# Performance work log

Measured on AMD Instinct MI355X. Metric: run time of the kernel, lower is better.

Reference implementation:

```python
import jax, jax.numpy as jnp
import numpy as np

# Model hyperparameters (from init_kwargs)
B, N, D = 64, 196, 768      # batch, patches, patch_dim
TKN = 768                   # token dim
QK = 64                     # per-head qk dim
H = 12                      # heads
HN = int(4.0 * TKN)         # Hopfield hidden = 3072
BETA = 1.0 / np.sqrt(QK)    # attn_beta default: 1/sqrt(qk_dim)
BLOCKS = 2
K_STEPS = 4                 # time_steps per block
EPS = 1e-5
ALPHA_RAW0 = float(np.log(np.exp(1.0) - 1.0))  # softplus^-1(alpha_init=1.0)


def setup_inputs() -> dict:
    key = jax.random.key(0)
    ks = jax.random.split(key, 8)
    sd = 0.02
    return {
        "x": jax.random.normal(ks[0], (B, N, D), dtype=jnp.float32),
        "W_enc": jax.random.normal(ks[1], (D, TKN), dtype=jnp.float32) * sd,
        "b_enc": jnp.zeros((TKN,), jnp.float32),
        "cls": jnp.ones((1, 1, TKN), jnp.float32),
        "pos": jax.random.normal(ks[2], (1, N + 1, TKN), dtype=jnp.float32) * sd,
        "gamma": jnp.ones((BLOCKS,), jnp.float32),             # EnergyLayerNorm scalar gain per block
        "bias": jnp.zeros((BLOCKS, TKN), jnp.float32),          # EnergyLayerNorm bias per block
        "Wq": jax.random.normal(ks[3], (BLOCKS, H, QK, TKN), dtype=jnp.float32) * sd,
        "Wk": jax.random.normal(ks[4], (BLOCKS, H, QK, TKN), dtype=jnp.float32) * sd,
        "Whn": jax.random.normal(ks[5], (BLOCKS, TKN, HN), dtype=jnp.float32) * sd,
        "alpha_raw": jnp.full((BLOCKS,), ALPHA_RAW0, jnp.float32),
        "ln_g": jnp.ones((TKN,), jnp.float32),
        "ln_b": jnp.zeros((TKN,), jnp.float32),
        "W_dec": jax.random.normal(ks[6], (TKN, D), dtype=jnp.float32) * sd,
        "b_dec": jnp.zeros((D,), jnp.float32),
    }


def _enorm(x, g_scale, g_bias):
    # EnergyLayerNorm: scalar gamma, per-dim bias, RMS of centered x
    xm = x - x.mean(-1, keepdims=True)
    return g_scale * xm * jax.lax.rsqrt((xm * xm).mean(-1, keepdims=True) + EPS) + g_bias


def _energy(g, Wq, Wk, Whn):
    # Hopfield-attention energy: -1/beta * sum logsumexp(beta * K^T Q)
    q = jnp.einsum("bnd,hzd->bnhz", g, Wq)
    k = jnp.einsum("bnd,hzd->bnhz", g, Wk)
    logits = jnp.einsum("bqhz,bkhz->bhqk", q, k)  # [B,H,N+1,N+1]
    e_attn = -(1.0 / BETA) * jnp.sum(jax.nn.logsumexp(BETA * logits, axis=-1))
    # Hopfield memory energy: -0.5 * sum relu(g W)^2
    e_hn = -0.5 * jnp.sum(jax.nn.relu(g @ Whn) ** 2)
    return e_attn + e_hn


_egrad = jax.grad(_energy)


def reference(x, W_enc, b_enc, cls, pos, gamma, bias, Wq, Wk, Whn, alpha_raw,
              ln_g, ln_b, W_dec, b_dec):
    t = x @ W_enc + b_enc                                   # encode -> [B,N,TKN]
    t = jnp.concatenate([jnp.broadcast_to(cls, (t.shape[0], 1, TKN)), t], axis=1)
    t = t + pos                                             # [B,N+1,TKN]
    for b in range(BLOCKS):
        a = jax.nn.softplus(alpha_raw[b])
        for _ in range(K_STEPS):
            g = _enorm(t, gamma[b], bias[b])
            t = t - a * _egrad(g, Wq[b], Wk[b], Whn[b])
    # decode: standard LayerNorm then Linear
    mu = t.mean(-1, keepdims=True)
    var = ((t - mu) ** 2).mean(-1, keepdims=True)
    h = (t - mu) * jax.lax.rsqrt(var + EPS) * ln_g + ln_b
    out = h @ W_dec + b_dec
    return out[:, 1:]                                       # drop CLS -> [B,N,D]
```

## Files before the change

kernel.cpp:

```cpp
#include <hip/hip_runtime.h>
#include <cstdint>
#include <cstddef>

using u16 = unsigned short;
typedef short short8 __attribute__((ext_vector_type(8)));
typedef short short4v __attribute__((ext_vector_type(4)));
typedef float f32x4 __attribute__((ext_vector_type(4)));

#define LN_EPS 1e-5f
#define ATT_BETA 0.125f

__device__ __forceinline__ u16 f2bf(float f){
  uint32_t u = __float_as_uint(f);
  u += 0x7fffu + ((u >> 16) & 1u);
  return (u16)(u >> 16);
}
__device__ __forceinline__ float bf2f(u16 h){
  return __uint_as_float(((uint32_t)h) << 16);
}
__device__ __forceinline__ float wred_sum(float v){
  #pragma unroll
  for(int o=32;o;o>>=1) v += __shfl_xor(v,o,64);
  return v;
}
__device__ __forceinline__ void async16(const void* g, void* l){
  __builtin_amdgcn_global_load_lds((const __attribute__((address_space(1))) void*)g,
                                   (__attribute__((address_space(3))) void*)l, 16, 0, 0);
}

template<int EPI, int ASPL>
__global__ __launch_bounds__(256)
void gemm_bt(const u16* __restrict__ A, const u16* __restrict__ A2,
             const u16* __restrict__ B,
             u16* __restrict__ Cb, float* __restrict__ Cf,
             int M, int N, int K, int ldb, int ldc,
             const float* __restrict__ aux0, const float* __restrict__ aux1,
             const float* __restrict__ araw, int blk)
{
  __shared__ u16 lA[128*32];
  __shared__ u16 lB[128*32];
  int tid = threadIdx.x;
  int w = tid >> 6, l = tid & 63;
  int wm = w >> 1, wn = w & 1;
  int m0 = blockIdx.y * 128, n0 = blockIdx.x * 128;
  int lr = l >> 2;
  int lc = (l & 3) * 8;
  f32x4 acc[4][4];
  #pragma unroll
  for(int i=0;i<4;i++)
    #pragma unroll
    for(int j=0;j<4;j++) acc[i][j] = (f32x4){0.f,0.f,0.f,0.f};
  int fm = l & 15, fq = (l >> 4) * 8;

  for(int kt=0; kt<K; kt+=32){
    __syncthreads();
    const u16* Asrc = A; int kcol = kt;
    if(ASPL){ if(kt >= 768){ Asrc = A2; kcol = kt - 768; } }
    int lda = ASPL ? 768 : K;
    #pragma unroll
    for(int c=0;c<2;c++){
      int rr = (w*2+c)*16;
      int ga = m0 + rr + lr; if(ga > M-1) ga = M-1;
      async16(Asrc + (size_t)ga*lda + kcol + lc, &lA[rr*32]);
      int gb = n0 + rr + lr; if(gb > N-1) gb = N-1;
      async16(B + (size_t)gb*ldb + kt + lc, &lB[rr*32]);
    }
    __syncthreads();
    short8 af[4], bfv[4];
    #pragma unroll
    for(int i=0;i<4;i++) af[i]  = *(const short8*)&lA[(wm*64 + i*16 + fm)*32 + fq];
    #pragma unroll
    for(int j=0;j<4;j++) bfv[j] = *(const short8*)&lB[(wn*64 + j*16 + fm)*32 + fq];
    #pragma unroll
    for(int i=0;i<4;i++)
      #pragma unroll
      for(int j=0;j<4;j++)
        acc[i][j] = __builtin_amdgcn_mfma_f32_16x16x32_bf16(af[i], bfv[j], acc[i][j], 0, 0, 0);
  }

  float alpha = 0.f;
  if(EPI==2) alpha = log1pf(__expf(araw[blk]));

  #pragma unroll
  for(int i=0;i<4;i++){
    int row_b = m0 + wm*64 + i*16 + (l>>4)*4;
    #pragma unroll
    for(int j=0;j<4;j++){
      int col = n0 + wn*64 + j*16 + (l&15);
      #pragma unroll
      for(int r=0;r<4;r++){
        int row = row_b + r;
        if(row >= M) continue;
        float v = acc[i][j][r];
        if(EPI==1){
          Cb[(size_t)row*ldc + col] = f2bf(v > 0.f ? v : 0.f);
        } else if(EPI==2){
          Cf[(size_t)row*768 + col] += alpha * v;
        } else if(EPI==3){
          int pb = row / 196, pn = row - pb*196;
          Cf[((size_t)pb*197 + 1 + pn)*768 + col] = v + aux0[col] + aux1[(size_t)(1+pn)*768 + col];
        } else {
          int pb = row / 197, rr2 = row - pb*197;
          if(rr2 > 0) Cf[((size_t)pb*196 + rr2 - 1)*768 + col] = v + aux0[col];
        }
      }
    }
  }
}

__global__ __launch_bounds__(256)
void norm_k(const float* __restrict__ t, u16* __restrict__ out,
            const float* __restrict__ gv, const float* __restrict__ bv, int blk, int mode)
{
  __shared__ float r1[4], r2[4];
  int row = blockIdx.x;
  const float* tr = t + (size_t)row*768;
  int tid = threadIdx.x, w = tid>>6, l = tid&63;
  f32x4 v = (f32x4){0.f,0.f,0.f,0.f};
  float s=0.f, s2=0.f;
  if(tid < 192){
    v = ((const f32x4*)tr)[tid];
    s  = v[0]+v[1]+v[2]+v[3];
    s2 = v[0]*v[0]+v[1]*v[1]+v[2]*v[2]+v[3]*v[3];
  }
  s = wred_sum(s); s2 = wred_sum(s2);
  if(l==0){ r1[w]=s; r2[w]=s2; }
  __syncthreads();
  s  = r1[0]+r1[1]+r1[2]+r1[3];
  s2 = r2[0]+r2[1]+r2[2]+r2[3];
  float mu  = s * (1.0f/768.0f);
  float var = s2 * (1.0f/768.0f) - mu*mu;
  float rs  = rsqrtf(var + LN_EPS);
  u16* orow = out + (size_t)row*768;
  if(tid < 192){
    short4v o;
    if(mode==0){
      float gm = gv[blk];
      const float* bb = bv + blk*768;
      #pragma unroll
      for(int c=0;c<4;c++) o[c] = (short)f2bf((v[c]-mu)*rs*gm + bb[tid*4+c]);
    } else {
      #pragma unroll
      for(int c=0;c<4;c++) o[c] = (short)f2bf((v[c]-mu)*rs*gv[tid*4+c] + bv[tid*4+c]);
    }
    ((short4v*)orow)[tid] = o;
  }
}

__global__ __launch_bounds__(512, 2)
void attn_fused(const u16* __restrict__ g, const u16* __restrict__ Wqk,
                u16* __restrict__ GqO, u16* __restrict__ GkO)
{
  __shared__ u16 smem[76800];
  __shared__ float SredS[2][4][16];
  u16* Qlds = smem;
  u16* Klds = smem + 14976;
  u16* QTl  = smem + 29952;
  u16* KTl  = smem + 44800;
  u16* P    = smem + 59648;
  u16* PT   = smem + 67840;
  u16* lg   = smem + 59648;

  int bhw = blockIdx.x;
  int bh = (bhw & 7)*96 + (bhw >> 3);
  int b = bh/12, h = bh - b*12;
  const u16* grows = g + (size_t)b*197*768;
  u16* Qg = GqO + (size_t)b*197*768 + h*64;
  u16* Kg = GkO + (size_t)b*197*768 + h*64;
  int tid = threadIdx.x, w = tid>>6, l = tid&63;
  int lane16 = l & 15, quad = l >> 4;

  for(int idx=tid; idx<64*24; idx+=512){
    int z = idx/24, c = 208 + (idx - (idx/24)*24);
    QTl[z*232 + c] = 0; KTl[z*232 + c] = 0;
  }

  {
    int half = w >> 2;
    int wsub = w & 3;
    int rt0 = (wsub==0) ? 0 : 1 + 3*wsub;
    int rtn = (wsub==0) ? 4 : 3;
    const u16* Wb = Wqk + (size_t)half*589824 + (size_t)(h*64)*768;
    u16* Lr = half ? Klds : Qlds;
    u16* Lt = half ? KTl  : QTl;
    f32x4 acc[4][4];
    #pragma unroll
    for(int i=0;i<4;i++)
      #pragma unroll
      for(int z=0;z<4;z++) acc[i][z] = (f32x4){0.f,0.f,0.f,0.f};

    int c40 = tid/208,        r0a = tid - c40*208;        int rr0 = r0a>196?196:r0a;
    int t1  = tid + 512;
    int c41 = t1/208,         r1a = t1  - c41*208;        int rr1 = r1a>196?196:r1a;
    #define STAGE_G(bufi, ktv) do{                                                     \
      async16(grows + (size_t)rr0*768 + (ktv)*32 + c40*8, lg + (bufi)*6656 + tid*8);   \
      if(t1 < 832)                                                                     \
        async16(grows + (size_t)rr1*768 + (ktv)*32 + c41*8, lg + (bufi)*6656 + t1*8);  \
    }while(0)

    short8 bq[4], bqn[4];
    #pragma unroll
    for(int z=0;z<4;z++) bq[z] = *(const short8*)(Wb + (size_t)(z*16+lane16)*768 + quad*8);
    STAGE_G(0, 0);
    int buf = 0;
    for(int kt=0; kt<24; kt++){
      __syncthreads();
      if(kt < 23){
        STAGE_G(buf^1, kt+1);
        #pragma unroll
        for(int z=0;z<4;z++)
          bqn[z] = *(const short8*)(Wb + (size_t)(z*16+lane16)*768 + (kt+1)*32 + quad*8);
      }
      const u16* lb = lg + buf*6656;
      #pragma unroll
      for(int i=0;i<4;i++) if(i<rtn){
        short8 af = *(const short8*)(lb + ((size_t)(quad*208 + (rt0+i)*16 + lane16))*8);
        #pragma unroll
        for(int z=0;z<4;z++)
          acc[i][z] = __builtin_amdgcn_mfma_f32_16x16x32_bf16(af, bq[z], acc[i][z],0,0,0);
      }
      #pragma unroll
      for(int z=0;z<4;z++) bq[z] = bqn[z];
      buf ^= 1;
    }
    #undef STAGE_G

    #pragma unroll
    for(int i=0;i<4;i++) if(i<rtn)
      #pragma unroll
      for(int z=0;z<4;z++)
        #pragma unroll
        for(int r=0;r<4;r++){
          int q  = (rt0+i)*16 + quad*4 + r;
          int zz = z*16 + lane16;
          u16 hv = f2bf(acc[i][z][r]);
          Lr[q*72   + zz] = hv;
          Lt[zz*232 + q ] = hv;
        }
  }
  __syncthreads();

  {
    int q = tid>>4, j = 208 + (tid&15);
    P[q*256 + 8*((j>>3)^(q&7)) + (j&7)] = 0;
  }

  int mt = w & 1, nh = w >> 1;
  int ncnt = (nh==0) ? 4 : 3;
  int nt0s = (nh==0) ? 0 : (1 + 3*nh);
  int jt0 = (w<5) ? 2*w : 10+(w-5);
  int jn  = (w<5) ? 2 : 1;

  f32x4 gk[2][4];
  #pragma unroll
  for(int a=0;a<2;a++)
    #pragma unroll
    for(int n2=0;n2<4;n2++) gk[a][n2] = (f32x4){0.f,0.f,0.f,0.f};

  for(int st=0; st<7; st++){
    int q0 = st*32;
    __syncthreads();
    int qa = q0 + 16*mt + lane16; if(qa > 196) qa = 196;
    short8 a0 = *(const short8*)&Qlds[qa*72 + quad*8];
    short8 a1 = *(const short8*)&Qlds[qa*72 + 32 + quad*8];
    f32x4 sa[4];
    #pragma unroll
    for(int ni=0;ni<4;ni++) sa[ni] = (f32x4){0.f,0.f,0.f,0.f};
    for(int ni=0; ni<ncnt; ni++){
      int jb = (nt0s+ni)*16 + lane16; if(jb > 196) jb = 196;
      short8 b0 = *(const short8*)&Klds[jb*72 + quad*8];
      short8 b1 = *(const short8*)&Klds[jb*72 + 32 + quad*8];
      sa[ni] = __builtin_amdgcn_mfma_f32_16x16x32_bf16(a0, b0, sa[ni],0,0,0);
      sa[ni] = __builtin_amdgcn_mfma_f32_16x16x32_bf16(a1, b1, sa[ni],0,0,0);
    }
    for(int ni=0; ni<ncnt; ni++){
      if((nt0s+ni)*16 + lane16 > 196){
        sa[ni][0]=-3e38f; sa[ni][1]=-3e38f; sa[ni][2]=-3e38f; sa[ni][3]=-3e38f;
      }
    }
    float ss[4] = {0.f,0.f,0.f,0.f};
    for(int ni=0; ni<ncnt; ni++)
      #pragma unroll
      for(int r=0;r<4;r++){
        float e = __expf(fminf(ATT_BETA*sa[ni][r], 80.f));
        sa[ni][r] = e; ss[r] += e;
      }
    #pragma unroll
    for(int o=1;o<16;o<<=1)
      #pragma unroll
      for(int r=0;r<4;r++) ss[r] += __shfl_xor(ss[r], o, 64);
    if(lane16==0){
      #pragma unroll
      for(int r=0;r<4;r++) SredS[mt][nh][quad*4+r] = ss[r];
    }
    __syncthreads();
    float inv[4];
    #pragma unroll
    for(int r=0;r<4;r++)
      inv[r] = 1.f/(SredS[mt][0][quad*4+r] + SredS[mt][1][quad*4+r]
                  + SredS[mt][2][quad*4+r] + SredS[mt][3][quad*4+r]);
    for(int ni=0; ni<ncnt; ni++){
      int j = (nt0s+ni)*16 + lane16;
      short4v pk;
      #pragma unroll
      for(int r=0;r<4;r++){
        int q = 16*mt + quad*4 + r;
        float val = (q0 + q <= 196) ? sa[ni][r]*inv[r] : 0.f;
        u16 hv = f2bf(val);
        P[q*256 + 8*((j>>3)^(q&7)) + (j&7)] = hv;
        pk[r] = (short)hv;
      }
      *(short4v*)&PT[j*40 + 16*mt + 4*quad] = pk;
    }
    __syncthreads();
    {
      f32x4 gq = (f32x4){0.f,0.f,0.f,0.f};
      int qrow = 16*mt + lane16;
      int z = nh*16 + lane16;
      for(int kt=0; kt<7; kt++){
        short8 af = *(const short8*)&P[qrow*256 + 8*((4*kt+quad)^(qrow&7))];
        short8 bf8 = *(const short8*)&KTl[z*232 + kt*32 + quad*8];
        gq = __builtin_amdgcn_mfma_f32_16x16x32_bf16(af, bf8, gq,0,0,0);
      }
      #pragma unroll
      for(int r=0;r<4;r++){
        int qg2 = q0 + 16*mt + quad*4 + r;
        if(qg2 <= 196) Qg[(size_t)qg2*768 + nh*16 + lane16] = f2bf(gq[r]);
      }
    }
    {
      short8 bq2[4];
      #pragma unroll
      for(int n2=0;n2<4;n2++)
        bq2[n2] = *(const short8*)&QTl[(n2*16+lane16)*232 + q0 + quad*8];
      for(int ji=0; ji<jn; ji++){
        int j = (jt0+ji)*16 + lane16;
        short8 af = *(const short8*)&PT[j*40 + quad*8];
        #pragma unroll
        for(int n2=0;n2<4;n2++)
          gk[ji][n2] = __builtin_amdgcn_mfma_f32_16x16x32_bf16(af, bq2[n2], gk[ji][n2],0,0,0);
      }
    }
  }
  __syncthreads();
  for(int ji=0; ji<jn; ji++){
    int jt = jt0 + ji;
    #pragma unroll
    for(int n2=0;n2<4;n2++)
      #pragma unroll
      for(int r=0;r<4;r++){
        int j = jt*16 + quad*4 + r;
        if(j <= 196) Kg[(size_t)j*768 + n2*16 + lane16] = f2bf(gk[ji][n2][r]);
      }
  }
}

__global__ void cvt_k(const float* __restrict__ in, u16* __restrict__ out, int n){
  for(int i=blockIdx.x*256+threadIdx.x; i<n; i+=gridDim.x*256) out[i] = f2bf(in[i]);
}

__global__ __launch_bounds__(256)
void tr_k(const float* __restrict__ src, u16* __restrict__ dst, int R, int C, int dstride, int coff){
  __shared__ float tile[32][33];
  int c0 = blockIdx.x*32, r0 = blockIdx.y*32;
  int tx = threadIdx.x & 31, ty = threadIdx.x >> 5;
  for(int i=ty;i<32;i+=8) tile[i][tx] = src[(size_t)(r0+i)*C + c0 + tx];
  __syncthreads();
  for(int i=ty;i<32;i+=8) dst[(size_t)(c0+i)*dstride + coff + r0 + tx] = f2bf(tile[tx][i]);
}

__global__ void fill_cls_k(float* __restrict__ t, const float* __restrict__ cls, const float* __restrict__ pos){
  int b = blockIdx.x;
  for(int i=threadIdx.x;i<768;i+=256) t[(size_t)b*197*768 + i] = cls[i] + pos[i];
}

extern "C" void kernel_launch(void* const* d_in, const int* in_sizes, int n_in,
                              void* d_out, int out_size, void* d_ws, size_t ws_size,
                              hipStream_t stream){
  const float* x      = (const float*)d_in[0];
  const float* W_enc  = (const float*)d_in[1];
  const float* b_enc  = (const float*)d_in[2];
  const float* cls    = (const float*)d_in[3];
  const float* pos    = (const float*)d_in[4];
  const float* gamma  = (const float*)d_in[5];
  const float* bias   = (const float*)d_in[6];
  const float* Wq     = (const float*)d_in[7];
  const float* Wk     = (const float*)d_in[8];
  const float* Whn    = (const float*)d_in[9];
  const float* araw   = (const float*)d_in[10];
  const float* ln_g   = (const float*)d_in[11];
  const float* ln_b   = (const float*)d_in[12];
  const float* W_dec  = (const float*)d_in[13];
  const float* b_dec  = (const float*)d_in[14];
  float* out = (float*)d_out;
  (void)in_sizes; (void)n_in; (void)out_size;

  const int M  = 64*197;
  const int MX = 64*196;

  char* p = (char*)d_ws;
  float* t   = (float*)p;  p += (size_t)M*768*4;
  u16*   g   = (u16*)p;    p += (size_t)M*768*2;
  u16*   Qb  = (u16*)p;    p += (size_t)M*768*2;
  u16*   Kb  = (u16*)p;    p += (size_t)M*768*2;
  size_t base = (size_t)(p - (char*)d_ws);
  if(base > ws_size) return;
  u16* hidden; int hop_merged;
  if(base + (size_t)M*3072*2 <= ws_size){ hidden = (u16*)(d_ws) + base/2; hop_merged = 1; }
  else { hidden = Qb; hop_merged = 0; }

  u16* Wall = (u16*)d_out;
  u16* Wqkb = Wall;
  u16* WqkT = Wall + 2359296;
  u16* WhnT = Wall + 4718592;
  u16* WhnB = Wall + 9437184;
  u16* xb    = Qb;
  u16* WencT = Kb;
  u16* WdecT = Kb;

  for(int b=0;b<2;b++){
    cvt_k<<<512,256,0,stream>>>(Wq + (size_t)b*589824, Wqkb + (size_t)b*1179648, 589824);
    cvt_k<<<512,256,0,stream>>>(Wk + (size_t)b*589824, Wqkb + (size_t)b*1179648 + 589824, 589824);
    tr_k<<<dim3(24,24),256,0,stream>>>(Wq + (size_t)b*589824, WqkT + (size_t)b*1179648, 768,768, 1536, 0);
    tr_k<<<dim3(24,24),256,0,stream>>>(Wk + (size_t)b*589824, WqkT + (size_t)b*1179648, 768,768, 1536, 768);
    tr_k<<<dim3(96,24),256,0,stream>>>(Whn + (size_t)b*2359296, WhnT + (size_t)b*2359296, 768,3072, 768, 0);
    cvt_k<<<2048,256,0,stream>>>(Whn + (size_t)b*2359296, WhnB + (size_t)b*2359296, 2359296);
  }

  cvt_k<<<1024,256,0,stream>>>(x, xb, MX*768);
  tr_k<<<dim3(24,24),256,0,stream>>>(W_enc, WencT, 768,768, 768, 0);
  fill_cls_k<<<64,256,0,stream>>>(t, cls, pos);
  gemm_bt<3,0><<<dim3(6,98),256,0,stream>>>(xb, nullptr, WencT, nullptr, t,
                                            MX, 768, 768, 768, 768,
                                            b_enc, pos, nullptr, 0);

  for(int blk=0; blk<2; blk++){
    for(int s=0; s<4; s++){
      norm_k<<<M,256,0,stream>>>(t, g, gamma, bias, blk, 0);
      if(hop_merged){
        gemm_bt<1,0><<<dim3(24,99),256,0,stream>>>(g, nullptr,
            WhnT + (size_t)blk*2359296,
            hidden, nullptr, M, 3072, 768, 768, 3072,
            nullptr, nullptr, nullptr, 0);
        gemm_bt<2,0><<<dim3(6,99),256,0,stream>>>(hidden, nullptr,
            WhnB + (size_t)blk*2359296,
            nullptr, t, M, 768, 3072, 3072, 768,
            nullptr, nullptr, araw, blk);
      } else {
        for(int c=0;c<2;c++){
          gemm_bt<1,0><<<dim3(12,99),256,0,stream>>>(g, nullptr,
              WhnT + (size_t)blk*2359296 + (size_t)c*1536*768,
              hidden, nullptr, M, 1536, 768, 768, 1536,
              nullptr, nullptr, nullptr, 0);
          gemm_bt<2,0><<<dim3(6,99),256,0,stream>>>(hidden, nullptr,
              WhnB + (size_t)blk*2359296 + (size_t)c*1536,
              nullptr, t, M, 768, 1536, 3072, 768,
              nullptr, nullptr, araw, blk);
        }
      }
      attn_fused<<<768,512,0,stream>>>(g, Wqkb + (size_t)blk*1179648, Qb, Kb);
      gemm_bt<2,1><<<dim3(6,99),256,0,stream>>>(Qb, Kb, WqkT + (size_t)blk*1179648,
            nullptr, t, M, 768, 1536, 1536, 768,
            nullptr, nullptr, araw, blk);
    }
  }

  tr_k<<<dim3(24,24),256,0,stream>>>(W_dec, WdecT, 768,768, 768, 0);
  norm_k<<<M,256,0,stream>>>(t, g, ln_g, ln_b, 0, 1);
  gemm_bt<4,0><<<dim3(6,99),256,0,stream>>>(g, nullptr, WdecT, nullptr, out,
                                            M, 768, 768, 768, 768,
                                            b_dec, nullptr, nullptr, 0);
}
```

Measured before the change: 4.290 ms.

## Swizzle GEMM workgroups per XCD, coalesce QK staging, drop loop barrier

The GEMM block index is remapped so consecutive tiles land on the same XCD, which should improve L2 reuse of A and B rows. The Q/K projection staging in the attention kernel changes its LDS layout from column-major chunks to row-major 4x16B per row, giving more contiguous global loads at the cost of a different LDS read pattern that may bank-conflict. A __syncthreads at the top of the score loop is removed, which cuts barrier overhead but risks a race if the later code reuses shared buffers across iterations.

Result: faster. 4.031 ms (-6.0%).

```diff
diff --git a/kernel.cpp b/kernel.cpp
--- a/kernel.cpp
+++ b/kernel.cpp
@@ -42,7 +42,11 @@
   int tid = threadIdx.x;
   int w = tid >> 6, l = tid & 63;
   int wm = w >> 1, wn = w & 1;
-  int m0 = blockIdx.y * 128, n0 = blockIdx.x * 128;
+  unsigned nwg = gridDim.x*gridDim.y;
+  unsigned lin = blockIdx.y*gridDim.x + blockIdx.x;
+  unsigned qq = nwg>>3, rr = nwg&7, xcd = lin&7, idx = lin>>3;
+  unsigned swz = (xcd<rr ? xcd*(qq+1) : rr*(qq+1) + (xcd-rr)*qq) + idx;
+  int m0 = (int)(swz / gridDim.x) * 128, n0 = (int)(swz % gridDim.x) * 128;
   int lr = l >> 2;
   int lc = (l & 3) * 8;
   f32x4 acc[4][4];
@@ -59,11 +63,11 @@
     int lda = ASPL ? 768 : K;
     #pragma unroll
     for(int c=0;c<2;c++){
-      int rr = (w*2+c)*16;
-      int ga = m0 + rr + lr; if(ga > M-1) ga = M-1;
-      async16(Asrc + (size_t)ga*lda + kcol + lc, &lA[rr*32]);
-      int gb = n0 + rr + lr; if(gb > N-1) gb = N-1;
-      async16(B + (size_t)gb*ldb + kt + lc, &lB[rr*32]);
+      int rr2 = (w*2+c)*16;
+      int ga = m0 + rr2 + lr; if(ga > M-1) ga = M-1;
+      async16(Asrc + (size_t)ga*lda + kcol + lc, &lA[rr2*32]);
+      int gb = n0 + rr2 + lr; if(gb > N-1) gb = N-1;
+      async16(B + (size_t)gb*ldb + kt + lc, &lB[rr2*32]);
     }
     __syncthreads();
     short8 af[4], bfv[4];
@@ -100,8 +104,8 @@
           int pb = row / 196, pn = row - pb*196;
           Cf[((size_t)pb*197 + 1 + pn)*768 + col] = v + aux0[col] + aux1[(size_t)(1+pn)*768 + col];
         } else {
-          int pb = row / 197, rr2 = row - pb*197;
-          if(rr2 > 0) Cf[((size_t)pb*196 + rr2 - 1)*768 + col] = v + aux0[col];
+          int pb = row / 197, rr3 = row - pb*197;
+          if(rr3 > 0) Cf[((size_t)pb*196 + rr3 - 1)*768 + col] = v + aux0[col];
         }
       }
     }
@@ -189,13 +193,12 @@
       #pragma unroll
       for(int z=0;z<4;z++) acc[i][z] = (f32x4){0.f,0.f,0.f,0.f};
 
-    int c40 = tid/208,        r0a = tid - c40*208;        int rr0 = r0a>196?196:r0a;
-    int t1  = tid + 512;
-    int c41 = t1/208,         r1a = t1  - c41*208;        int rr1 = r1a>196?196:r1a;
-    #define STAGE_G(bufi, ktv) do{                                                     \
-      async16(grows + (size_t)rr0*768 + (ktv)*32 + c40*8, lg + (bufi)*6656 + tid*8);   \
-      if(t1 < 832)                                                                     \
-        async16(grows + (size_t)rr1*768 + (ktv)*32 + c41*8, lg + (bufi)*6656 + t1*8);  \
+    #define STAGE_G(bufi, ktv) do{                                                    \
+      { int rw = tid>>2, c4 = tid&3; int r2 = rw>196?196:rw;                          \
+        async16(grows + (size_t)r2*768 + (ktv)*32 + c4*8, lg + (bufi)*6656 + tid*8);} \
+      int i1 = tid + 512;                                                             \
+      if(i1 < 832){ int rw = i1>>2, c4 = i1&3; int r2 = rw>196?196:rw;                \
+        async16(grows + (size_t)r2*768 + (ktv)*32 + c4*8, lg + (bufi)*6656 + i1*8);}  \
     }while(0)
 
     short8 bq[4], bqn[4];
@@ -214,7 +217,7 @@
       const u16* lb = lg + buf*6656;
       #pragma unroll
       for(int i=0;i<4;i++) if(i<rtn){
-        short8 af = *(const short8*)(lb + ((size_t)(quad*208 + (rt0+i)*16 + lane16))*8);
+        short8 af = *(const short8*)(lb + (size_t)((rt0+i)*16 + lane16)*32 + quad*8);
         #pragma unroll
         for(int z=0;z<4;z++)
           acc[i][z] = __builtin_amdgcn_mfma_f32_16x16x32_bf16(af, bq[z], acc[i][z],0,0,0);
@@ -259,7 +262,6 @@
 
   for(int st=0; st<7; st++){
     int q0 = st*32;
-    __syncthreads();
     int qa = q0 + 16*mt + lane16; if(qa > 196) qa = 196;
     short8 a0 = *(const short8*)&Qlds[qa*72 + quad*8];
     short8 a1 = *(const short8*)&Qlds[qa*72 + 32 + quad*8];
```
